# Kernel optimization log

Measured on AMD Instinct MI355X. Metric: run time of the kernel, lower is better.

Reference implementation:

```python
import jax, jax.numpy as jnp
import numpy as np

B = 16
TOP_N = 4
IOU_THRESH = 0.25
PAD = 224
OUT = 224  # part image size
NUM_CLASSES = 200


def _gen_anchors(input_shape=(448, 448)):
    # Faithful port of NTSNet._generate_default_anchor_maps -> edge anchors,
    # then +PAD shift and int cast as in NTSNet.__init__.
    scales = [2.0 ** (1.0 / 3.0), 2.0 ** (2.0 / 3.0)]
    ratios = [0.667, 1.0, 1.5]
    settings = [(32, 48, scales), (64, 96, scales), (128, 192, [1.0] + scales)]
    edge = []
    for stride, size, scs in settings:
        H = int(np.ceil(input_shape[0] / stride))
        W = int(np.ceil(input_shape[1] / stride))
        ostart = stride / 2.0
        oy = np.arange(ostart, ostart + stride * H, stride).reshape(H, 1)
        ox = np.arange(ostart, ostart + stride * W, stride).reshape(1, W)
        cy = np.broadcast_to(oy, (H, W)).astype(np.float32)
        cx = np.broadcast_to(ox, (H, W)).astype(np.float32)
        for s in scs:
            for ar in ratios:
                h = size * s / float(ar) ** 0.5
                w = size * s * float(ar) ** 0.5
                e = np.stack([cy - h / 2.0, cx - w / 2.0, cy + h / 2.0, cx + w / 2.0], axis=-1)
                edge.append(e.reshape(-1, 4))
    edge = np.concatenate(edge, axis=0).astype(np.float32)
    return (edge + PAD).astype(np.int64).astype(np.int32)  # [1614,4] (y0,x0,y1,x1)


def _conv(x, w, b, stride, pad):
    y = jax.lax.conv_general_dilated(
        x, w, window_strides=(stride, stride),
        padding=[(pad, pad), (pad, pad)],
        dimension_numbers=("NCHW", "OIHW", "NCHW"))
    return y + b[None, :, None, None]


def _nms_single(scores, boxes, areas):
    # Hard NMS, fixed TOP_N iterations (jit-friendly): iteratively take the
    # highest-score box and suppress boxes with IoU >= IOU_THRESH.
    valid = jnp.ones(scores.shape, dtype=bool)
    picked = []
    for _ in range(TOP_N):
        i = jnp.argmax(jnp.where(valid, scores, -jnp.inf))
        b = boxes[i]
        ih = jnp.minimum(boxes[:, 2], b[2]) - jnp.maximum(boxes[:, 0], b[0])
        iw = jnp.minimum(boxes[:, 3], b[3]) - jnp.maximum(boxes[:, 1], b[1])
        inter = jnp.where((ih < 0) | (iw < 0), 0.0, ih * iw)
        iou = inter / (areas + areas[i] - inter)
        valid = valid & (iou < IOU_THRESH)
        picked.append(i)
    return jnp.stack(picked)  # [TOP_N]


def _crop_resize(img, box):
    # Bilinear resize of img[:, y0:y1, x0:x1] to OUTxOUT, align_corners=True
    # (matches F.interpolate(..., mode='bilinear', align_corners=True)).
    y0, x0, y1, x1 = box[0], box[1], box[2], box[3]
    h = (y1 - y0).astype(jnp.float32)
    w = (x1 - x0).astype(jnp.float32)
    t = jnp.arange(OUT, dtype=jnp.float32)
    sy = t * (h - 1.0) / (OUT - 1.0)
    sx = t * (w - 1.0) / (OUT - 1.0)
    fy = jnp.floor(sy)
    fx = jnp.floor(sx)
    wy = (sy - fy)[None, :, None]  # broadcast over rows
    wx = (sx - fx)[None, None, :]  # broadcast over cols
    iy0 = y0 + fy.astype(jnp.int32)
    ix0 = x0 + fx.astype(jnp.int32)
    iy1 = jnp.minimum(iy0 + 1, y1 - 1)
    ix1 = jnp.minimum(ix0 + 1, x1 - 1)
    r0 = img[:, iy0]  # [3,OUT,896]
    r1 = img[:, iy1]
    top = r0[:, :, ix0] * (1.0 - wx) + r0[:, :, ix1] * wx
    bot = r1[:, :, ix0] * (1.0 - wx) + r1[:, :, ix1] * wx
    return top * (1.0 - wy) + bot * wy  # [3,OUT,OUT]


def setup_inputs() -> dict:
    key = jax.random.key(0)
    ks = jax.random.split(key, 10)
    s = 0.02
    inp = {
        "x": jax.random.normal(ks[0], (B, 3, 448, 448), jnp.float32),
        "bb_w": jax.random.normal(ks[1], (2048, 3, 32, 32), jnp.float32) * s,
        "bb_b": jnp.zeros((2048,), jnp.float32),
        "n1_dw": jax.random.normal(ks[2], (128, 2048, 3, 3), jnp.float32) * s,
        "n1_db": jnp.zeros((128,), jnp.float32),
        "n1_tw": jax.random.normal(ks[3], (6, 128, 1, 1), jnp.float32) * s,
        "n1_tb": jnp.zeros((6,), jnp.float32),
        "n2_dw": jax.random.normal(ks[4], (128, 128, 3, 3), jnp.float32) * s,
        "n2_db": jnp.zeros((128,), jnp.float32),
        "n2_tw": jax.random.normal(ks[5], (6, 128, 1, 1), jnp.float32) * s,
        "n2_tb": jnp.zeros((6,), jnp.float32),
        "n3_dw": jax.random.normal(ks[6], (128, 128, 3, 3), jnp.float32) * s,
        "n3_db": jnp.zeros((128,), jnp.float32),
        "n3_tw": jax.random.normal(ks[7], (9, 128, 1, 1), jnp.float32) * s,
        "n3_tb": jnp.zeros((9,), jnp.float32),
        "cn_w": jax.random.normal(ks[8], (NUM_CLASSES, 10240), jnp.float32) * s,
        "cn_b": jnp.zeros((NUM_CLASSES,), jnp.float32),
        "anchors": jnp.asarray(_gen_anchors()),
    }
    return inp


def reference(x, bb_w, bb_b, n1_dw, n1_db, n1_tw, n1_tb, n2_dw, n2_db, n2_tw,
              n2_tb, n3_dw, n3_db, n3_tw, n3_tb, cn_w, cn_b, anchors):
    batch = x.shape[0]
    # Backbone -> raw pre-features [B,2048,14,14]
    raw = _conv(x, bb_w, bb_b, stride=32, pad=0)
    # Navigator unit -> rpn scores [B,1614]
    y1 = jax.nn.relu(_conv(raw, n1_dw, n1_db, 1, 1))            # [B,128,14,14]
    t1 = _conv(y1, n1_tw, n1_tb, 1, 0).reshape(batch, -1)        # [B,1176]
    y2 = jax.nn.relu(_conv(y1, n2_dw, n2_db, 2, 1))              # [B,128,7,7]
    t2 = _conv(y2, n2_tw, n2_tb, 1, 0).reshape(batch, -1)        # [B,294]
    y3 = jax.nn.relu(_conv(y2, n3_dw, n3_db, 2, 1))              # [B,128,4,4]
    t3 = _conv(y3, n3_tw, n3_tb, 1, 0).reshape(batch, -1)        # [B,144]
    rpn_score = jnp.concatenate([t1, t2, t3], axis=1)            # [B,1614]

    boxes_f = anchors.astype(jnp.float32)
    areas = (boxes_f[:, 2] - boxes_f[:, 0]) * (boxes_f[:, 3] - boxes_f[:, 1])
    top_idx = jax.vmap(_nms_single, in_axes=(0, None, None))(rpn_score, boxes_f, areas)  # [B,TOP_N]

    x_pad = jnp.pad(x, ((0, 0), (0, 0), (PAD, PAD), (PAD, PAD)))  # [B,3,896,896]
    sel_boxes = anchors[top_idx]                                  # [B,TOP_N,4]
    part_imgs = jax.vmap(lambda img, bs: jax.vmap(_crop_resize, in_axes=(None, 0))(img, bs))(
        x_pad, sel_boxes)                                         # [B,TOP_N,3,224,224]
    part_imgs = jax.lax.stop_gradient(part_imgs).reshape(batch * TOP_N, 3, OUT, OUT)

    # Shared backbone + tail (global avg pool; dropout is identity in eval)
    part_features = _conv(part_imgs, bb_w, bb_b, 32, 0).mean(axis=(2, 3))  # [B*TOP_N,2048]
    part_feature = part_features.reshape(batch, TOP_N, -1)[:, :4].reshape(batch, -1)  # num_cat=4
    raw_features = jax.lax.stop_gradient(raw).mean(axis=(2, 3))            # [B,2048]

    concat_out = jnp.concatenate([part_feature, raw_features], axis=1)     # [B,10240]
    concat_logits = concat_out @ cn_w.T + cn_b
    return concat_logits
```

## Files before the change

kernel.cpp:

```cpp
#include <hip/hip_runtime.h>
#include <cstdint>
#include <math.h>

typedef _Float16 half_t;
typedef __attribute__((ext_vector_type(8))) _Float16 half8;
typedef __attribute__((ext_vector_type(4))) float floatx4;


typedef __attribute__((address_space(3))) unsigned int lds_u32;
typedef const __attribute__((address_space(1))) unsigned int glb_u32;
__device__ __forceinline__ void glds16(const void* g, void* l) {
    __builtin_amdgcn_global_load_lds((glb_u32*)g, (lds_u32*)l, 16, 0, 0);
}

__global__ __launch_bounds__(256)
void prep_all(const float* __restrict__ x, const float* __restrict__ bbw,
              const float* __restrict__ n1dw, const float* __restrict__ n2dw,
              const float* __restrict__ n3dw, const float* __restrict__ cnb,
              const float* __restrict__ bbb,
              half_t* __restrict__ xh,
              half_t* __restrict__ bh, half_t* __restrict__ w1h,
              float* __restrict__ wt2t, float* __restrict__ wt3t,
              float* __restrict__ out, float* __restrict__ zpad,
              float* __restrict__ concat)
{
    const int t = blockIdx.x * 256 + threadIdx.x;
    if (t < 307200) {
        const int m = t % 3200, s = t / 3200;
        const int mt = m >> 7, mr = m & 127;
        float f[32];
        if (m < 3136) {
            const int bq = m / 196, pos = m % 196, oy = pos / 14, ox = pos % 14;
            const int c = s >> 5, r = s & 31;
            const float* p = x + ((size_t)(bq * 3 + c) * 448 + oy * 32 + r) * 448 + ox * 32;
            #pragma unroll
            for (int i = 0; i < 8; ++i) *(float4*)&f[i * 4] = *(const float4*)(p + i * 4);
        } else {
            #pragma unroll
            for (int j = 0; j < 32; ++j) f[j] = 0.f;
        }
        #pragma unroll
        for (int kg = 0; kg < 4; ++kg) {
            half8 h;
            #pragma unroll
            for (int j = 0; j < 8; ++j) h[j] = (half_t)f[kg * 8 + j];
            const size_t dst = (((size_t)(mt * 96 + s) * 4 + kg) * 128 + mr) * 8;
            *(half8*)(xh + dst) = h;
        }
    } else if (t < 503808) {
        const int t2 = t - 307200;
        const int n = t2 & 2047, s = t2 >> 11;
        const float* p = bbw + (size_t)n * 3072 + s * 32;
        float f[32];
        #pragma unroll
        for (int i = 0; i < 8; ++i) *(float4*)&f[i * 4] = *(const float4*)(p + i * 4);
        const int nt = n >> 6, nr = n & 63;
        #pragma unroll
        for (int kg = 0; kg < 4; ++kg) {
            half8 h;
            #pragma unroll
            for (int j = 0; j < 8; ++j) h[j] = (half_t)f[kg * 8 + j];
            const size_t dst = (((size_t)(nt * 96 + s) * 4 + kg) * 64 + nr) * 8;
            *(half8*)(bh + dst) = h;
        }
    } else if (t < 536576) {
        const int t2 = t - 503808;
        const int n = t2 >> 8, ic8 = t2 & 255;
        const int s = ic8 >> 2, kg = ic8 & 3;
        const float* src = n1dw + ((size_t)n * 2048 + ic8 * 8) * 9;
        float buf[72];
        #pragma unroll
        for (int i = 0; i < 18; ++i) *(float4*)&buf[i * 4] = *(const float4*)(src + i * 4);
        #pragma unroll
        for (int tap = 0; tap < 9; ++tap) {
            half8 h;
            #pragma unroll
            for (int j = 0; j < 8; ++j) h[j] = (half_t)buf[j * 9 + tap];
            const size_t dst = (((size_t)(tap * 64 + s) * 4 + kg) * 128 + n) * 8;
            *(half8*)(w1h + dst) = h;
        }
    } else if (t < 684032) {
        const int t2 = t - 536576;
        const int oc = t2 % 128, rest = t2 / 128, ic = rest % 128, tap = rest / 128;
        wt2t[(tap * 128 + ic) * 128 + oc] = n2dw[((size_t)oc * 128 + ic) * 9 + tap];
    } else if (t < 831488) {
        const int t2 = t - 684032;
        const int oc = t2 % 128, rest = t2 / 128, ic = rest % 128, tap = rest / 128;
        wt3t[(tap * 128 + ic) * 128 + oc] = n3dw[((size_t)oc * 128 + ic) * 9 + tap];
    } else if (t < 834688) {
        const int i = t - 831488;
        out[i] = cnb[i % 200];
    } else if (t < 834944) {
        zpad[t - 834688] = 0.f;
    } else if (t < 998784) {
        const int i = t - 834944;
        const int r = i % 10240;
        concat[i] = (r < 8192) ? bbb[r & 2047] : 0.f;
    }
}

__global__ __launch_bounds__(256)
void gemm_x(const half_t* __restrict__ Ah, const half_t* __restrict__ Bh,
            const float* __restrict__ bias, half_t* __restrict__ outh)
{
    __shared__ __align__(16) char L[49152];
    const int tid = threadIdx.x, lane = tid & 63, wv = tid >> 6;
    const int bid = blockIdx.y * 16 + blockIdx.x;
    const int swz = (bid & 7) * 98 + (bid >> 3);
    const int nt = swz & 15, mt = swz >> 4;
    const int lm = lane & 15, quad = lane >> 4;

    const char* gA = (const char*)Ah + (size_t)(mt >> 1) * 786432 + (mt & 1) * 1024 + lane * 16;
    const char* gB = (const char*)Bh + (size_t)(2 * nt) * 393216 + lane * 16;

    const int a0 = 2 * wv, a1 = 2 * wv + 1;
    const int aof0 = (a0 >> 2) * 4096 + (a0 & 3) * 1024;
    const int aog0 = (a0 >> 2) * 8192 + (a0 & 3) * 2048;
    const int aof1 = (a1 >> 2) * 4096 + (a1 & 3) * 1024;
    const int aog1 = (a1 >> 2) * 8192 + (a1 & 3) * 2048;
    const int bsi = wv >> 1, bnh = wv & 1;
    const size_t bgb = (size_t)bnh * 393216 + bsi * 4096;
    const int blb = 8192 + (bsi * 2 + bnh) * 4096;

    floatx4 acc[8];
    const floatx4 fz = {0.f, 0.f, 0.f, 0.f};
    #pragma unroll
    for (int j = 0; j < 8; ++j) acc[j] = fz;

    glds16(gA + aog0, L + aof0);
    glds16(gA + aog1, L + aof1);
    #pragma unroll
    for (int i = 0; i < 4; ++i)
        glds16(gB + bgb + i * 1024, L + blb + i * 1024);
    asm volatile("s_waitcnt vmcnt(0)" ::: "memory");
    __builtin_amdgcn_s_barrier();

    for (int s = 0; s < 48; ++s) {
        const char* Lc = L + (s & 1) * 24576;
        char* Ln = L + ((s + 1) & 1) * 24576;
        if (s < 47) {
            const size_t sa = (size_t)(2 * (s + 1)) * 8192;
            const size_t sb = (size_t)(2 * (s + 1)) * 4096;
            glds16(gA + sa + aog0, Ln + aof0);
            glds16(gA + sa + aog1, Ln + aof1);
            #pragma unroll
            for (int i = 0; i < 4; ++i)
                glds16(gB + bgb + sb + i * 1024, Ln + blb + i * 1024);
        }
        #pragma unroll
        for (int ki = 0; ki < 2; ++ki) {
            half8 a = *(const half8*)(Lc + ki * 4096 + quad * 1024 + (wv * 16 + lm) * 16);
            #pragma unroll
            for (int j = 0; j < 8; ++j) {
                half8 b = *(const half8*)(Lc + 8192 + (ki * 2 + (j >> 2)) * 4096 + quad * 1024 + ((j & 3) * 16 + lm) * 16);
                acc[j] = __builtin_amdgcn_mfma_f32_16x16x32_f16(a, b, acc[j], 0, 0, 0);
            }
        }
        asm volatile("s_waitcnt vmcnt(0) lgkmcnt(0)" ::: "memory");
        __builtin_amdgcn_s_barrier();
    }
    const int m0 = mt * 64 + wv * 16 + quad * 4;
    #pragma unroll
    for (int j = 0; j < 8; ++j) {
        const int n = nt * 128 + j * 16 + lm;
        const float bv = bias[n];
        #pragma unroll
        for (int r = 0; r < 4; ++r)
            outh[(size_t)(m0 + r) * 2048 + n] = (half_t)(acc[j][r] + bv);
    }
}

__global__ __launch_bounds__(256)
void gemm_nav(const half_t* __restrict__ rawh, const half_t* __restrict__ Bh,
              const char* __restrict__ zpad, float* __restrict__ y1p)
{
    __shared__ __align__(16) char L[49152];
    const int tid = threadIdx.x, lane = tid & 63, wv = tid >> 6;
    const int bid = blockIdx.y * 18 + blockIdx.x;
    const int xcd = bid & 7, ii = bid >> 3;
    const int swz = (xcd < 2 ? xcd * 111 : 222 + (xcd - 2) * 110) + ii;
    const int tx = swz % 18, mt = swz / 18;
    const int tap = tx >> 1, ks = tx & 1;
    const int lm = lane & 15, quad = lane >> 4;

    const int grow = mt * 64 + lane;
    const int b = grow / 196, pos = grow % 196, oy = pos / 14, ox = pos % 14;
    const int iy = oy + tap / 3 - 1, ix = ox + tap % 3 - 1;
    const bool av = (iy >= 0 && iy < 14 && ix >= 0 && ix < 14);
    const char* abase = av ? (const char*)rawh + ((size_t)(b * 196 + iy * 14 + ix)) * 4096 + ks * 2048 : zpad;
    const int stp = av ? 1 : 0;

    const int a0 = 2 * wv, a1 = 2 * wv + 1;
    const int ac0 = (a0 >> 2) * 64 + (a0 & 3) * 16, al0 = (a0 >> 2) * 4096 + (a0 & 3) * 1024;
    const int ac1 = (a1 >> 2) * 64 + (a1 & 3) * 16, al1 = (a1 >> 2) * 4096 + (a1 & 3) * 1024;
    const int bsi = wv >> 1, bnh = wv & 1;
    const char* gB = (const char*)Bh + (size_t)tap * 524288 + (size_t)(ks * 32) * 8192 + bnh * 1024 + lane * 16;
    const int blb = 8192 + bsi * 8192 + bnh * 1024;

    floatx4 acc[8];
    const floatx4 fz = {0.f, 0.f, 0.f, 0.f};
    #pragma unroll
    for (int j = 0; j < 8; ++j) acc[j] = fz;

    glds16(abase + stp * ac0, L + al0);
    glds16(abase + stp * ac1, L + al1);
    {
        const size_t sb0 = (size_t)bsi * 8192;
        #pragma unroll
        for (int i = 0; i < 4; ++i)
            glds16(gB + sb0 + i * 2048, L + blb + i * 2048);
    }
    asm volatile("s_waitcnt vmcnt(0)" ::: "memory");
    __builtin_amdgcn_s_barrier();

    for (int s = 0; s < 16; ++s) {
        const char* Lc = L + (s & 1) * 24576;
        char* Ln = L + ((s + 1) & 1) * 24576;
        if (s < 15) {
            const int rowo = (s + 1) * 128;
            glds16(abase + stp * (rowo + ac0), Ln + al0);
            glds16(abase + stp * (rowo + ac1), Ln + al1);
            const size_t sb = (size_t)(2 * (s + 1) + bsi) * 8192;
            #pragma unroll
            for (int i = 0; i < 4; ++i)
                glds16(gB + sb + i * 2048, Ln + blb + i * 2048);
        }
        #pragma unroll
        for (int ki = 0; ki < 2; ++ki) {
            half8 a = *(const half8*)(Lc + ki * 4096 + quad * 1024 + (wv * 16 + lm) * 16);
            #pragma unroll
            for (int j = 0; j < 8; ++j) {
                half8 bq = *(const half8*)(Lc + 8192 + ki * 8192 + quad * 2048 + (j * 16 + lm) * 16);
                acc[j] = __builtin_amdgcn_mfma_f32_16x16x32_f16(a, bq, acc[j], 0, 0, 0);
            }
        }
        asm volatile("s_waitcnt vmcnt(0) lgkmcnt(0)" ::: "memory");
        __builtin_amdgcn_s_barrier();
    }
    const int m0 = mt * 64 + wv * 16 + quad * 4;
    #pragma unroll
    for (int j = 0; j < 8; ++j) {
        const int n = j * 16 + lm;
        #pragma unroll
        for (int r = 0; r < 4; ++r)
            y1p[((size_t)tx * 3136 + m0 + r) * 128 + n] = acc[j][r];
    }
}

__global__ __launch_bounds__(256)
void y1r_rm(const float* __restrict__ y1p, const float* __restrict__ bias,
            float* __restrict__ y1,
            const half_t* __restrict__ rh, float* __restrict__ concat)
{
    if (blockIdx.x < 1568) {
        const int t = blockIdx.x * 256 + threadIdx.x;
        const int n = t & 127;
        float s = bias[n];
        #pragma unroll
        for (int ks = 0; ks < 18; ++ks) s += y1p[(size_t)ks * 3136 * 128 + t];
        y1[t] = fmaxf(s, 0.f);
    } else {
        const int t = (blockIdx.x - 1568) * 256 + threadIdx.x;
        const int n = t & 2047, b = (t >> 11) & 15, pc = t >> 15;
        float s = 0.f;
        const int p0 = pc * 49;
        for (int p = p0; p < p0 + 49; ++p)
            s += (float)rh[(size_t)(b * 196 + p) * 2048 + n];
        atomicAdd(concat + (size_t)b * 10240 + 8192 + n, s * (1.f / 196.f));
    }
}

__device__ __forceinline__ void tidy_one(const float* in, const float* wr, float bi,
                                         float* dst, int lane)
{
    float acc = in[lane] * wr[lane] + in[lane + 64] * wr[lane + 64];
    #pragma unroll
    for (int s = 32; s > 0; s >>= 1) acc += __shfl_down(acc, s, 64);
    if (lane == 0) *dst = acc + bi;
}

__device__ __forceinline__ void conv_s2_body(int t, const float* __restrict__ in,
                                             const float* __restrict__ wt,
                                             const float* __restrict__ bias,
                                             float* __restrict__ out, int Win, int Wout)
{
    const int oc = t & 127;
    const int pos = (t >> 7) % (Wout * Wout);
    const int b = t / (128 * Wout * Wout);
    if (b >= 16) return;
    const int oy = pos / Wout, ox = pos % Wout;
    float acc = bias[oc];
    for (int dy = 0; dy < 3; ++dy) {
        const int y = oy * 2 + dy - 1;
        if (y < 0 || y >= Win) continue;
        for (int dx = 0; dx < 3; ++dx) {
            const int x = ox * 2 + dx - 1;
            if (x < 0 || x >= Win) continue;
            const float* ip = in + (size_t)(b * Win * Win + y * Win + x) * 128;
            const float* wp = wt + (size_t)(dy * 3 + dx) * 16384 + oc;
            for (int ic = 0; ic < 128; ++ic)
                acc += ip[ic] * wp[ic * 128];
        }
    }
    out[(size_t)(b * Wout * Wout + pos) * 128 + oc] = fmaxf(acc, 0.f);
}

__global__ __launch_bounds__(256)
void conv2_tidy1(const float* __restrict__ y1, const float* __restrict__ wt2t,
                 const float* __restrict__ b2d, float* __restrict__ y2,
                 const float* __restrict__ w1t, const float* __restrict__ b1t,
                 float* __restrict__ scores)
{
    if (blockIdx.x < 392) {
        conv_s2_body(blockIdx.x * 256 + threadIdx.x, y1, wt2t, b2d, y2, 14, 7);
    } else {
        const int wid = (blockIdx.x - 392) * 4 + (threadIdx.x >> 6);
        const int lane = threadIdx.x & 63;
        if (wid >= 16 * 1176) return;
        const int b = wid / 1176, i1 = wid % 1176;
        const int ch = i1 / 196, pos = i1 % 196;
        tidy_one(y1 + (size_t)(b * 196 + pos) * 128, w1t + ch * 128, b1t[ch],
                 scores + b * 1614 + i1, lane);
    }
}

__global__ __launch_bounds__(256)
void conv3_tidy2(const float* __restrict__ y2, const float* __restrict__ wt3t,
                 const float* __restrict__ b3d, float* __restrict__ y3,
                 const float* __restrict__ w2t, const float* __restrict__ b2t,
                 float* __restrict__ scores)
{
    if (blockIdx.x < 128) {
        conv_s2_body(blockIdx.x * 256 + threadIdx.x, y2, wt3t, b3d, y3, 7, 4);
    } else {
        const int wid = (blockIdx.x - 128) * 4 + (threadIdx.x >> 6);
        const int lane = threadIdx.x & 63;
        if (wid >= 16 * 294) return;
        const int b = wid / 294, i2 = wid % 294;
        const int ch = i2 / 49, pos = i2 % 49;
        tidy_one(y2 + (size_t)(b * 49 + pos) * 128, w2t + ch * 128, b2t[ch],
                 scores + b * 1614 + 1176 + i2, lane);
    }
}

__global__ __launch_bounds__(256)
void tidy3(const float* __restrict__ y3, const float* __restrict__ w3t,
           const float* __restrict__ b3t, float* __restrict__ scores)
{
    const int wid = blockIdx.x * 4 + (threadIdx.x >> 6);
    const int lane = threadIdx.x & 63;
    if (wid >= 16 * 144) return;
    const int b = wid / 144, i3 = wid % 144;
    const int ch = i3 / 16, pos = i3 % 16;
    tidy_one(y3 + (size_t)(b * 16 + pos) * 128, w3t + ch * 128, b3t[ch],
             scores + b * 1614 + 1470 + i3, lane);
}

__global__ __launch_bounds__(256)
void nms(const float* __restrict__ scores, const int* __restrict__ anchors,
         int* __restrict__ top_idx)
{
    __shared__ float wv_v[4];
    __shared__ int wv_i[4];
    __shared__ int s_pick;
    const int b = blockIdx.x, tid = threadIdx.x;
    const int lane = tid & 63, wv = tid >> 6;
    float sc[7], ay0[7], ax0[7], ay1[7], ax1[7];
    unsigned int vmask = 0;
    #pragma unroll
    for (int j = 0; j < 7; ++j) {
        const int i = tid + j * 256;
        if (i < 1614) {
            sc[j]  = scores[b * 1614 + i];
            ay0[j] = (float)anchors[i * 4 + 0];
            ax0[j] = (float)anchors[i * 4 + 1];
            ay1[j] = (float)anchors[i * 4 + 2];
            ax1[j] = (float)anchors[i * 4 + 3];
            vmask |= 1u << j;
        }
    }
    for (int r = 0; r < 4; ++r) {
        float bv = -INFINITY; int bi = 0x7fffffff;
        #pragma unroll
        for (int j = 0; j < 7; ++j) {
            if (vmask & (1u << j)) {
                const float v = sc[j];
                const int i = tid + j * 256;
                if (v > bv || (v == bv && i < bi)) { bv = v; bi = i; }
            }
        }
        #pragma unroll
        for (int s = 32; s > 0; s >>= 1) {
            const float v2 = __shfl_down(bv, s, 64);
            const int   i2 = __shfl_down(bi, s, 64);
            if (v2 > bv || (v2 == bv && i2 < bi)) { bv = v2; bi = i2; }
        }
        if (lane == 0) { wv_v[wv] = bv; wv_i[wv] = bi; }
        __syncthreads();
        if (tid == 0) {
            float fv = wv_v[0]; int fi = wv_i[0];
            #pragma unroll
            for (int k = 1; k < 4; ++k)
                if (wv_v[k] > fv || (wv_v[k] == fv && wv_i[k] < fi)) { fv = wv_v[k]; fi = wv_i[k]; }
            s_pick = fi;
            top_idx[b * 4 + r] = fi;
        }
        __syncthreads();
        const int pick = s_pick;
        const float py0 = (float)anchors[pick * 4 + 0], px0 = (float)anchors[pick * 4 + 1];
        const float py1 = (float)anchors[pick * 4 + 2], px1 = (float)anchors[pick * 4 + 3];
        const float pa = (py1 - py0) * (px1 - px0);
        #pragma unroll
        for (int j = 0; j < 7; ++j) {
            if (vmask & (1u << j)) {
                const float ih = fminf(ay1[j], py1) - fmaxf(ay0[j], py0);
                const float iw = fminf(ax1[j], px1) - fmaxf(ax0[j], px0);
                const float inter = (ih < 0.f || iw < 0.f) ? 0.f : ih * iw;
                const float area = (ay1[j] - ay0[j]) * (ax1[j] - ax0[j]);
                const float iou = inter / ((area + pa) - inter);
                if (iou >= 0.25f) vmask &= ~(1u << j);
            }
        }
    }
}

__global__ __launch_bounds__(256)
void crop_mean(const float* __restrict__ x, const int* __restrict__ anchors,
               const int* __restrict__ top_idx, float* __restrict__ abar)
{
    __shared__ float red[256];
    const int bi = blockIdx.x;
    const int q = bi / 96, rem = bi % 96, c = rem >> 5, r = rem & 31;
    const int tid = threadIdx.x;
    const int cc = tid & 31, ps = tid >> 5;
    const int idx = top_idx[q];
    const int y0 = anchors[idx * 4 + 0], x0 = anchors[idx * 4 + 1];
    const int y1 = anchors[idx * 4 + 2], x1 = anchors[idx * 4 + 3];
    const float hh = (float)(y1 - y0), ww = (float)(x1 - x0);
    const float* xb = x + (size_t)((q >> 2) * 3 + c) * 200704;
    float acc = 0.f;
    for (int p = ps; p < 49; p += 8) {
        const int oy = p / 7, ox = p % 7;
        const int typ = oy * 32 + r;
        const int txp = ox * 32 + cc;
        const float sy = (float)typ * (hh - 1.0f) / 223.0f;
        const float fy = floorf(sy);
        const float wy = sy - fy;
        const int iy0 = y0 + (int)fy;
        const int iy1 = min(iy0 + 1, y1 - 1);
        const float sx = (float)txp * (ww - 1.0f) / 223.0f;
        const float fx = floorf(sx);
        const float wx = sx - fx;
        const int ix0 = x0 + (int)fx;
        const int ix1 = min(ix0 + 1, x1 - 1);
        const int ry0 = iy0 - 224, ry1 = iy1 - 224;
        const int rx0 = ix0 - 224, rx1 = ix1 - 224;
        const bool vy0 = (ry0 >= 0 && ry0 < 448), vy1 = (ry1 >= 0 && ry1 < 448);
        const bool vx0 = (rx0 >= 0 && rx0 < 448), vx1 = (rx1 >= 0 && rx1 < 448);
        const float v00 = (vy0 && vx0) ? xb[(size_t)ry0 * 448 + rx0] : 0.f;
        const float v01 = (vy0 && vx1) ? xb[(size_t)ry0 * 448 + rx1] : 0.f;
        const float v10 = (vy1 && vx0) ? xb[(size_t)ry1 * 448 + rx0] : 0.f;
        const float v11 = (vy1 && vx1) ? xb[(size_t)ry1 * 448 + rx1] : 0.f;
        const float top = v00 * (1.f - wx) + v01 * wx;
        const float bot = v10 * (1.f - wx) + v11 * wx;
        acc += top * (1.f - wy) + bot * wy;
    }
    red[tid] = acc;
    __syncthreads();
    if (tid < 32) {
        float s = 0.f;
        #pragma unroll
        for (int k = 0; k < 8; ++k) s += red[tid + 32 * k];
        abar[(size_t)q * 3072 + c * 1024 + r * 32 + cc] = s * (1.f / 49.f);
    }
}

__global__ __launch_bounds__(256)
void part_gemm(const float* __restrict__ abar, const half_t* __restrict__ Bh,
               float* __restrict__ concat)
{
    __shared__ __align__(16) char L[12288];
    const int tid = threadIdx.x, lane = tid & 63, wv = tid >> 6;
    const int lm = lane & 15, quad = lane >> 4;
    const int nt = blockIdx.x, ks = blockIdx.y;
    const char* gBh = (const char*)Bh + ((size_t)nt * 96 + ks * 12) * 4096 + lane * 16;
    const int am = tid & 63, akg = tid >> 6;

    floatx4 acc[4], accl[4];
    const floatx4 fz = {0.f, 0.f, 0.f, 0.f};
    #pragma unroll
    for (int j = 0; j < 4; ++j) { acc[j] = fz; accl[j] = fz; }

    for (int s = 0; s < 12; ++s) {
        {
            const float* pa = abar + (size_t)am * 3072 + (ks * 12 + s) * 32 + akg * 8;
            float f[8];
            *(float4*)&f[0] = *(const float4*)pa;
            *(float4*)&f[4] = *(const float4*)(pa + 4);
            half8 h, l;
            #pragma unroll
            for (int j = 0; j < 8; ++j) {
                const half_t hh = (half_t)f[j];
                h[j] = hh;
                l[j] = (half_t)(f[j] - (float)hh);
            }
            *(half8*)(L + (akg * 64 + am) * 16) = h;
            *(half8*)(L + 4096 + (akg * 64 + am) * 16) = l;
        }
        glds16(gBh + (size_t)s * 4096 + wv * 1024, L + 8192 + wv * 1024);
        __syncthreads();
        half8 ah, al, bh[4];
        ah = *(const half8*)(L + (quad * 64 + wv * 16 + lm) * 16);
        al = *(const half8*)(L + 4096 + (quad * 64 + wv * 16 + lm) * 16);
        #pragma unroll
        for (int j = 0; j < 4; ++j) bh[j] = *(const half8*)(L + 8192 + (quad * 64 + j * 16 + lm) * 16);
        #pragma unroll
        for (int j = 0; j < 4; ++j) {
            acc[j]  = __builtin_amdgcn_mfma_f32_16x16x32_f16(ah, bh[j], acc[j], 0, 0, 0);
            accl[j] = __builtin_amdgcn_mfma_f32_16x16x32_f16(al, bh[j], accl[j], 0, 0, 0);
        }
        __syncthreads();
    }
    #pragma unroll
    for (int j = 0; j < 4; ++j) {
        const int n = nt * 64 + j * 16 + lm;
        #pragma unroll
        for (int r = 0; r < 4; ++r) {
            const int m = wv * 16 + quad * 4 + r;
            atomicAdd(concat + (size_t)(m >> 2) * 10240 + (m & 3) * 2048 + n,
                      acc[j][r] + accl[j][r]);
        }
    }
}

__global__ __launch_bounds__(256)
void cls_gemm(const float* __restrict__ concat, const float* __restrict__ w,
              float* __restrict__ out)
{
    __shared__ float ws_[8 * 321];
    __shared__ float cs_[16 * 321];
    __shared__ float red[256];
    const int nchunk = blockIdx.x, ks = blockIdx.y;
    const int tid = threadIdx.x;
    for (int i = tid; i < 2560; i += 256) {
        const int r = i / 320, k = i % 320;
        ws_[r * 321 + k] = w[(size_t)(nchunk * 8 + r) * 10240 + ks * 320 + k];
    }
    for (int i = tid; i < 5120; i += 256) {
        const int r = i / 320, k = i % 320;
        cs_[r * 321 + k] = concat[(size_t)r * 10240 + ks * 320 + k];
    }
    __syncthreads();
    const int b = tid & 15, c = (tid >> 4) & 7, hf = tid >> 7;
    const float* cp = cs_ + b * 321 + hf * 160;
    const float* wp = ws_ + c * 321 + hf * 160;
    float a = 0.f;
    #pragma unroll 8
    for (int k = 0; k < 160; ++k) a += cp[k] * wp[k];
    red[tid] = a;
    __syncthreads();
    if (tid < 128) atomicAdd(out + b * 200 + nchunk * 8 + c, red[tid] + red[tid + 128]);
}

extern "C" void kernel_launch(void* const* d_in, const int* in_sizes, int n_in,
                              void* d_out, int out_size, void* d_ws, size_t ws_size,
                              hipStream_t stream)
{
    const float* x     = (const float*)d_in[0];
    const float* bb_w  = (const float*)d_in[1];
    const float* bb_b  = (const float*)d_in[2];
    const float* n1_dw = (const float*)d_in[3];
    const float* n1_db = (const float*)d_in[4];
    const float* n1_tw = (const float*)d_in[5];
    const float* n1_tb = (const float*)d_in[6];
    const float* n2_dw = (const float*)d_in[7];
    const float* n2_db = (const float*)d_in[8];
    const float* n2_tw = (const float*)d_in[9];
    const float* n2_tb = (const float*)d_in[10];
    const float* n3_dw = (const float*)d_in[11];
    const float* n3_db = (const float*)d_in[12];
    const float* n3_tw = (const float*)d_in[13];
    const float* n3_tb = (const float*)d_in[14];
    const float* cn_w  = (const float*)d_in[15];
    const float* cn_b  = (const float*)d_in[16];
    const int*   anchors = (const int*)d_in[17];
    float* out = (float*)d_out;
    char* W = (char*)d_ws;

    half_t* bbwh  = (half_t*)(W + 0);
    float*  zpad  = (float*)(W + 12582912);
    int*    topidx= (int*)(W + 12583936);
    float*  scores= (float*)(W + 12584960);
    float*  y1    = (float*)(W + 12688384);
    float*  y2    = (float*)(W + 14294016);
    float*  y3    = (float*)(W + 14695424);
    float*  concat= (float*)(W + 14826496);
    half_t* w1h   = (half_t*)(W + 15481856);
    float*  wt2t  = (float*)(W + 20200448);
    float*  wt3t  = (float*)(W + 20790272);
    char* E = W + 21380096;
    half_t* xh    = (half_t*)E;
    float*  y1p   = (float*)E;
    char* F = W + 60701696;
    half_t* rawh  = (half_t*)F;
    float*  abar  = (float*)F;

    prep_all<<<3902, 256, 0, stream>>>(x, bb_w, n1_dw, n2_dw, n3_dw, cn_b, bb_b,
                                       xh, bbwh, w1h, wt2t, wt3t, out, zpad, concat);

    gemm_x<<<dim3(16, 49), 256, 0, stream>>>(xh, bbwh, bb_b, rawh);
    gemm_nav<<<dim3(18, 49), 256, 0, stream>>>(rawh, w1h, (const char*)zpad, y1p);
    y1r_rm<<<2080, 256, 0, stream>>>(y1p, n1_db, y1, rawh, concat);

    conv2_tidy1<<<5096, 256, 0, stream>>>(y1, wt2t, n2_db, y2, n1_tw, n1_tb, scores);
    conv3_tidy2<<<1304, 256, 0, stream>>>(y2, wt3t, n3_db, y3, n2_tw, n2_tb, scores);
    tidy3<<<576, 256, 0, stream>>>(y3, n3_tw, n3_tb, scores);

    nms<<<16, 256, 0, stream>>>(scores, anchors, topidx);
    crop_mean<<<6144, 256, 0, stream>>>(x, anchors, topidx, abar);

    part_gemm<<<dim3(32, 8), 256, 0, stream>>>(abar, bbwh, concat);
    cls_gemm<<<dim3(25, 32), 256, 0, stream>>>(concat, cn_w, out);
}
```

Measured before the change: 400.8 us.

## Load A fragments directly to registers and pipeline B via LDS with partial waits

In both GEMM kernels the A operand now goes straight from global memory into registers, double-buffered across steps, instead of being staged through LDS. Only B goes through LDS, which shrinks shared memory from 48KB to 32KB. The full vmcnt(0) wait is replaced by a partial vmcnt(6) wait, so the next tile's loads stay in flight during the MFMAs. The XCD-aware block swizzle is also dropped in favour of plain blockIdx mapping. This may lose L2 locality, and the vmcnt counting must line up with the exact load order to stay correct.

```diff
diff --git a/kernel.cpp b/kernel.cpp
--- a/kernel.cpp
+++ b/kernel.cpp
@@ -103,62 +103,61 @@
 void gemm_x(const half_t* __restrict__ Ah, const half_t* __restrict__ Bh,
             const float* __restrict__ bias, half_t* __restrict__ outh)
 {
-    __shared__ __align__(16) char L[49152];
+    __shared__ __align__(16) char L[32768];
     const int tid = threadIdx.x, lane = tid & 63, wv = tid >> 6;
-    const int bid = blockIdx.y * 16 + blockIdx.x;
-    const int swz = (bid & 7) * 98 + (bid >> 3);
-    const int nt = swz & 15, mt = swz >> 4;
+    const int nt = blockIdx.x, mt = blockIdx.y;
     const int lm = lane & 15, quad = lane >> 4;
 
-    const char* gA = (const char*)Ah + (size_t)(mt >> 1) * 786432 + (mt & 1) * 1024 + lane * 16;
+    const char* pA = (const char*)Ah + (size_t)(mt >> 1) * 786432 + (mt & 1) * 1024
+                   + quad * 2048 + (wv * 16 + lm) * 16;
     const char* gB = (const char*)Bh + (size_t)(2 * nt) * 393216 + lane * 16;
 
-    const int a0 = 2 * wv, a1 = 2 * wv + 1;
-    const int aof0 = (a0 >> 2) * 4096 + (a0 & 3) * 1024;
-    const int aog0 = (a0 >> 2) * 8192 + (a0 & 3) * 2048;
-    const int aof1 = (a1 >> 2) * 4096 + (a1 & 3) * 1024;
-    const int aog1 = (a1 >> 2) * 8192 + (a1 & 3) * 2048;
     const int bsi = wv >> 1, bnh = wv & 1;
     const size_t bgb = (size_t)bnh * 393216 + bsi * 4096;
-    const int blb = 8192 + (bsi * 2 + bnh) * 4096;
+    const int blb = (bsi * 2 + bnh) * 4096;
 
     floatx4 acc[8];
     const floatx4 fz = {0.f, 0.f, 0.f, 0.f};
     #pragma unroll
     for (int j = 0; j < 8; ++j) acc[j] = fz;
 
-    glds16(gA + aog0, L + aof0);
-    glds16(gA + aog1, L + aof1);
+    half8 aC0, aC1, aN0, aN1;
+
     #pragma unroll
     for (int i = 0; i < 4; ++i)
         glds16(gB + bgb + i * 1024, L + blb + i * 1024);
-    asm volatile("s_waitcnt vmcnt(0)" ::: "memory");
-    __builtin_amdgcn_s_barrier();
-
-    for (int s = 0; s < 48; ++s) {
-        const char* Lc = L + (s & 1) * 24576;
-        char* Ln = L + ((s + 1) & 1) * 24576;
-        if (s < 47) {
-            const size_t sa = (size_t)(2 * (s + 1)) * 8192;
-            const size_t sb = (size_t)(2 * (s + 1)) * 4096;
-            glds16(gA + sa + aog0, Ln + aof0);
-            glds16(gA + sa + aog1, Ln + aof1);
-            #pragma unroll
-            for (int i = 0; i < 4; ++i)
-                glds16(gB + bgb + sb + i * 1024, Ln + blb + i * 1024);
-        }
+    aC0 = *(const half8*)(pA);
+    aC1 = *(const half8*)(pA + 8192);
+
+    auto step = [&](int s, int sn, const char* Lc, char* Ln,
+                    half8& c0, half8& c1, half8& n0, half8& n1) {
+        #pragma unroll
+        for (int i = 0; i < 4; ++i)
+            glds16(gB + bgb + (size_t)sn * 8192 + i * 1024, Ln + blb + i * 1024);
+        n0 = *(const half8*)(pA + (size_t)sn * 16384);
+        n1 = *(const half8*)(pA + (size_t)sn * 16384 + 8192);
+        asm volatile("s_waitcnt vmcnt(6)" ::: "memory");
+        __builtin_amdgcn_s_barrier();
+        __builtin_amdgcn_sched_barrier(0);
         #pragma unroll
         for (int ki = 0; ki < 2; ++ki) {
-            half8 a = *(const half8*)(Lc + ki * 4096 + quad * 1024 + (wv * 16 + lm) * 16);
+            const half8 a = ki ? c1 : c0;
             #pragma unroll
             for (int j = 0; j < 8; ++j) {
-                half8 b = *(const half8*)(Lc + 8192 + (ki * 2 + (j >> 2)) * 4096 + quad * 1024 + ((j & 3) * 16 + lm) * 16);
+                half8 b = *(const half8*)(Lc + (ki * 2 + (j >> 2)) * 4096 + quad * 1024 + ((j & 3) * 16 + lm) * 16);
                 acc[j] = __builtin_amdgcn_mfma_f32_16x16x32_f16(a, b, acc[j], 0, 0, 0);
             }
         }
-        asm volatile("s_waitcnt vmcnt(0) lgkmcnt(0)" ::: "memory");
+        __builtin_amdgcn_sched_barrier(0);
         __builtin_amdgcn_s_barrier();
-    }
+    };
+
+    for (int h = 0; h < 24; ++h) {
+        const int s0 = 2 * h, s1 = 2 * h + 1;
+        step(s0, s0 + 1, L, L + 16384, aC0, aC1, aN0, aN1);
+        step(s1, (s1 < 47) ? s1 + 1 : 0, L + 16384, L, aN0, aN1, aC0, aC1);
+    }
+
     const int m0 = mt * 64 + wv * 16 + quad * 4;
     #pragma unroll
     for (int j = 0; j < 8; ++j) {
@@ -174,69 +173,67 @@
 void gemm_nav(const half_t* __restrict__ rawh, const half_t* __restrict__ Bh,
               const char* __restrict__ zpad, float* __restrict__ y1p)
 {
-    __shared__ __align__(16) char L[49152];
+    __shared__ __align__(16) char L[32768];
     const int tid = threadIdx.x, lane = tid & 63, wv = tid >> 6;
-    const int bid = blockIdx.y * 18 + blockIdx.x;
-    const int xcd = bid & 7, ii = bid >> 3;
-    const int swz = (xcd < 2 ? xcd * 111 : 222 + (xcd - 2) * 110) + ii;
-    const int tx = swz % 18, mt = swz / 18;
+    const int tx = blockIdx.x;
     const int tap = tx >> 1, ks = tx & 1;
+    const int mt = blockIdx.y;
     const int lm = lane & 15, quad = lane >> 4;
 
-    const int grow = mt * 64 + lane;
+    const int grow = mt * 64 + wv * 16 + lm;
     const int b = grow / 196, pos = grow % 196, oy = pos / 14, ox = pos % 14;
     const int iy = oy + tap / 3 - 1, ix = ox + tap % 3 - 1;
     const bool av = (iy >= 0 && iy < 14 && ix >= 0 && ix < 14);
-    const char* abase = av ? (const char*)rawh + ((size_t)(b * 196 + iy * 14 + ix)) * 4096 + ks * 2048 : zpad;
-    const int stp = av ? 1 : 0;
-
-    const int a0 = 2 * wv, a1 = 2 * wv + 1;
-    const int ac0 = (a0 >> 2) * 64 + (a0 & 3) * 16, al0 = (a0 >> 2) * 4096 + (a0 & 3) * 1024;
-    const int ac1 = (a1 >> 2) * 64 + (a1 & 3) * 16, al1 = (a1 >> 2) * 4096 + (a1 & 3) * 1024;
+    const char* fb = av ? (const char*)rawh + ((size_t)(b * 196 + iy * 14 + ix)) * 4096 + ks * 2048 : zpad;
+    const int fstp = av ? 1 : 0;
+    const char* fbase = fb + fstp * quad * 16;
+
     const int bsi = wv >> 1, bnh = wv & 1;
     const char* gB = (const char*)Bh + (size_t)tap * 524288 + (size_t)(ks * 32) * 8192 + bnh * 1024 + lane * 16;
-    const int blb = 8192 + bsi * 8192 + bnh * 1024;
+    const int blb = bsi * 8192 + bnh * 1024;
 
     floatx4 acc[8];
     const floatx4 fz = {0.f, 0.f, 0.f, 0.f};
     #pragma unroll
     for (int j = 0; j < 8; ++j) acc[j] = fz;
 
-    glds16(abase + stp * ac0, L + al0);
-    glds16(abase + stp * ac1, L + al1);
-    {
-        const size_t sb0 = (size_t)bsi * 8192;
+    half8 aC0, aC1, aN0, aN1;
+
+    #pragma unroll
+    for (int i = 0; i < 4; ++i)
+        glds16(gB + (size_t)bsi * 8192 + i * 2048, L + blb + i * 2048);
+    aC0 = *(const half8*)(fbase);
+    aC1 = *(const half8*)(fbase + fstp * 64);
+
+    auto step = [&](int s, int sn, const char* Lc, char* Ln,
+                    half8& c0, half8& c1, half8& n0, half8& n1) {
         #pragma unroll
         for (int i = 0; i < 4; ++i)
-            glds16(gB + sb0 + i * 2048, L + blb + i * 2048);
-    }
-    asm volatile("s_waitcnt vmcnt(0)" ::: "memory");
-    __builtin_amdgcn_s_barrier();
-
-    for (int s = 0; s < 16; ++s) {
-        const char* Lc = L + (s & 1) * 24576;
-        char* Ln = L + ((s + 1) & 1) * 24576;
-        if (s < 15) {
-            const int rowo = (s + 1) * 128;
-            glds16(abase + stp * (rowo + ac0), Ln + al0);
-            glds16(abase + stp * (rowo + ac1), Ln + al1);
-            const size_t sb = (size_t)(2 * (s + 1) + bsi) * 8192;
-            #pragma unroll
-            for (int i = 0; i < 4; ++i)
-                glds16(gB + sb + i * 2048, Ln + blb + i * 2048);
-        }
+            glds16(gB + (size_t)(2 * sn + bsi) * 8192 + i * 2048, Ln + blb + i * 2048);
+        n0 = *(const half8*)(fbase + fstp * (sn * 128));
+        n1 = *(const half8*)(fbase + fstp * (sn * 128 + 64));
+        asm volatile("s_waitcnt vmcnt(6)" ::: "memory");
+        __builtin_amdgcn_s_barrier();
+        __builtin_amdgcn_sched_barrier(0);
         #pragma unroll
         for (int ki = 0; ki < 2; ++ki) {
-            half8 a = *(const half8*)(Lc + ki * 4096 + quad * 1024 + (wv * 16 + lm) * 16);
+            const half8 a = ki ? c1 : c0;
             #pragma unroll
             for (int j = 0; j < 8; ++j) {
-                half8 bq = *(const half8*)(Lc + 8192 + ki * 8192 + quad * 2048 + (j * 16 + lm) * 16);
+                half8 bq = *(const half8*)(Lc + ki * 8192 + quad * 2048 + (j * 16 + lm) * 16);
                 acc[j] = __builtin_amdgcn_mfma_f32_16x16x32_f16(a, bq, acc[j], 0, 0, 0);
             }
         }
-        asm volatile("s_waitcnt vmcnt(0) lgkmcnt(0)" ::: "memory");
+        __builtin_amdgcn_sched_barrier(0);
         __builtin_amdgcn_s_barrier();
-    }
+    };
+
+    for (int h = 0; h < 8; ++h) {
+        const int s0 = 2 * h, s1 = 2 * h + 1;
+        step(s0, s0 + 1, L, L + 16384, aC0, aC1, aN0, aN1);
+        step(s1, (s1 < 15) ? s1 + 1 : 0, L + 16384, L, aN0, aN1, aC0, aC1);
+    }
+
     const int m0 = mt * 64 + wv * 16 + quad * 4;
     #pragma unroll
     for (int j = 0; j < 8; ++j) {
```

After: 380.5 us. 1.05x faster.
